# Optimization experiments

Hardware: AMD Instinct MI355X
Metric: run time of the kernel (lower is better)

Reference implementation:

```python
import jax, jax.numpy as jnp
from jax import lax
import numpy as np

T, B, H, D = 1024, 32, 8, 32
YD = 3 * D + 1
IN = H * D


def setup_inputs() -> dict:
    key = jax.random.key(0)
    ks = jax.random.split(key, 6)
    std = 1.0 / np.sqrt(D)
    return {
        "h": jax.random.normal(ks[0], (T, B, IN), jnp.float32),
        "W_y": (jax.random.normal(ks[1], (1, H, D, YD), jnp.float32) * std),
        "W_q": (jax.random.normal(ks[2], (1, H, D, D), jnp.float32) * std),
        "W_k": (jax.random.normal(ks[3], (1, H, D, D), jnp.float32) * std),
        "w_b": (jax.random.normal(ks[4], (1, H, D, 4), jnp.float32) * std),
        "W_out": (jax.random.normal(ks[5], (IN, IN), jnp.float32) / np.sqrt(IN)),
        "state_W_y": jnp.zeros((B, H, D, YD), jnp.float32),
        "state_W_q": jnp.zeros((B, H, D, D), jnp.float32),
        "state_W_k": jnp.zeros((B, H, D, D), jnp.float32),
        "state_w_b": jnp.zeros((B, H, D, 4), jnp.float32),
        "fast_weights": jnp.zeros((B, H, D, D), jnp.float32),
    }


def _srwm(x, Wy0, Wq0, Wk0, wb0):
    # Self-referential weight matrix (self_ref_v1): x time-major (T,B,H,D).
    def step(carry, x_t):
        Wy, Wq, Wk, wb = carry
        y = jnp.einsum('bhd,bhde->bhe', x_t, Wy)                      # output with W_{t-1}
        q = jax.nn.softmax(jnp.einsum('bhd,bhde->bhe', x_t, Wq), -1)
        k = jax.nn.softmax(jnp.einsum('bhd,bhde->bhe', x_t, Wk), -1)
        beta = jax.nn.sigmoid(jnp.einsum('bhd,bhde->bhe', x_t, wb))   # (B,H,4) learning rates
        def upd(M, b_i):
            vq = jnp.einsum('bhd,bhde->bhe', q, M)
            vk = jnp.einsum('bhd,bhde->bhe', k, M)
            return M + b_i[..., None, None] * k[..., :, None] * (vq - vk)[..., None, :]
        Wy = upd(Wy, beta[..., 0])
        Wq = upd(Wq, beta[..., 1])
        Wk = upd(Wk, beta[..., 2])
        wb = upd(wb, beta[..., 3])
        return (Wy, Wq, Wk, wb), y

    _, ys = lax.scan(step, (Wy0, Wq0, Wk0, wb0), x)
    return ys  # (T,B,H,YD)


def _fast_weight_memory(q, k, v, beta, F0):
    # Delta-rule fast weight memory; q,k,v (T,B,H,D), beta (T,B,H,1), F0 (B,H,D,D).
    def step(F, qkvb):
        q_t, k_t, v_t, b_t = qkvb
        v_old = jnp.einsum('bhd,bhde->bhe', k_t, F)
        F = F + b_t[..., None] * k_t[..., :, None] * (v_t - v_old)[..., None, :]
        out_t = jnp.einsum('bhd,bhde->bhe', q_t, F)
        return F, out_t

    F_fin, out = lax.scan(step, F0, (q, k, v, beta))
    return out, F_fin  # out: (T,B,H,D)


def reference(h, W_y, W_q, W_k, w_b, W_out,
              state_W_y, state_W_q, state_W_k, state_w_b, fast_weights):
    x = jax.nn.softmax(h.reshape(T, B, H, D), axis=-1)   # phi(x)
    Wy0 = state_W_y + W_y
    Wq0 = state_W_q + W_q
    Wk0 = state_W_k + W_k
    wb0 = state_w_b + w_b
    fast_qkvb = _srwm(x, Wy0, Wq0, Wk0, wb0)             # (T,B,H,3D+1)
    fq, fk, fv, fb = jnp.split(fast_qkvb, (D, 2 * D, 3 * D), axis=-1)
    fq = jax.nn.softmax(fq, -1)
    fk = jax.nn.softmax(fk, -1)
    fb = jax.nn.sigmoid(fb)
    out, _ = _fast_weight_memory(fq, fk, fv, fb, fast_weights)
    out = out.reshape(T, B, H * D)
    out = out @ W_out.T                                  # out_linear (no bias), dropout=0
    return h + out
```

## Files before the change

### kernel.cpp

```cpp
#include <hip/hip_runtime.h>
#include <cstdint>

#define TT  1024
#define BB  32
#define HH  8
#define DD  32
#define YDN 97
#define INN 256
#define BH  (BB*HH)

typedef float v2f __attribute__((ext_vector_type(2)));
typedef float v4f __attribute__((ext_vector_type(4)));

#define PK(acc, a, b) (acc) = __builtin_elementwise_fma((a), (b), (acc))

__device__ __forceinline__ void bar_lds() {
    asm volatile("s_waitcnt lgkmcnt(0)\n\ts_barrier" ::: "memory");
}
__device__ __forceinline__ void wait_lds() {
    asm volatile("s_waitcnt lgkmcnt(0)" ::: "memory");
}

template<int C>
__device__ __forceinline__ float dppf(float x) {
    return __int_as_float(__builtin_amdgcn_update_dpp(
        0, __float_as_int(x), C, 0xF, 0xF, true));
}
__device__ __forceinline__ float swz16(float x) {
    return __int_as_float(__builtin_amdgcn_ds_swizzle(__float_as_int(x), 0x401F));
}
__device__ __forceinline__ float xswap32(float v) {
    return __shfl_xor(v, 32, 64);
}
__device__ __forceinline__ float red_max32(float v) {
    v = fmaxf(v, dppf<0xB1>(v));
    v = fmaxf(v, dppf<0x4E>(v));
    v = fmaxf(v, dppf<0x141>(v));
    v = fmaxf(v, dppf<0x140>(v));
    v = fmaxf(v, swz16(v));
    return v;
}
__device__ __forceinline__ float red_sum32(float v) {
    v += dppf<0xB1>(v);
    v += dppf<0x4E>(v);
    v += dppf<0x141>(v);
    v += dppf<0x140>(v);
    v += swz16(v);
    return v;
}

__device__ __forceinline__ float cexp(float v) {
    return __expf(fminf(v, 60.f));
}

__device__ __forceinline__ float dot32(const v2f (&x)[16], const v2f (&w)[16]) {
    v2f a0 = {0.f, 0.f}, a1 = {0.f, 0.f};
    #pragma unroll
    for (int g = 0; g < 8; g++) {
        PK(a0, x[2*g],   w[2*g]);
        PK(a1, x[2*g+1], w[2*g+1]);
    }
    v2f s = a0 + a1;
    return s.x + s.y;
}

__device__ __forceinline__ void lds_read32x2(const float* a, const float* b,
                                             v2f (&ra)[16], v2f (&rb)[16]) {
    const v4f* ap = (const v4f*)a;
    const v4f* bp = (const v4f*)b;
    #pragma unroll
    for (int j = 0; j < 8; j++) {
        v4f x = ap[j]; ra[2*j] = x.xy; ra[2*j+1] = x.zw;
        v4f y = bp[j]; rb[2*j] = y.xy; rb[2*j+1] = y.zw;
    }
}

__device__ __forceinline__ void upd_row(v2f (&row2)[16], const float* u_p,
                                        const float* k_p, float beta) {
    v2f uu0[16], kk0[16];
    lds_read32x2(u_p, k_p, uu0, kk0);
    float du = dot32(uu0, row2);
    float bs = beta * du;
    v2f bs2 = {bs, bs};
    #pragma unroll
    for (int j = 0; j < 16; j++) PK(row2[j], bs2, kk0[j]);
}

__global__ __launch_bounds__(256, 1) void softmax_x_kernel(
    const float* __restrict__ hg, float* __restrict__ xg)
{
    const int row  = blockIdx.x * 8 + (threadIdx.x >> 5);
    const int lane = threadIdx.x & 31;
    float v = hg[(size_t)row * DD + lane];
    float m = red_max32(v);
    float ex = __expf(v - m);
    float sm = red_sum32(ex);
    xg[(size_t)row * DD + lane] = ex * __builtin_amdgcn_rcpf(sm);
}


#define PHASE_D(TP, P)                                                        \
    {                                                                         \
        const v4f* e4 = (const v4f*)exf_s[P];                                 \
        v2f fqh[8], fkh[8];                                                   \
        _Pragma("unroll")                                                     \
        for (int j = 0; j < 4; j++) {                                         \
            v4f a = e4[4*half + j];                                           \
            fqh[2*j] = a.xy; fqh[2*j+1] = a.zw;                               \
            v4f b = e4[8 + 4*half + j];                                       \
            fkh[2*j] = b.xy; fkh[2*j+1] = b.zw;                               \
        }                                                                     \
        float fvv = yv_s[P][l32];                                            \
        float fbp = yv_s[P][32];                                             \
                                     \
        v2f sq2 = {0.f,0.f}, sk2 = {0.f,0.f};                                 \
        _Pragma("unroll")                                                     \
        for (int j = 0; j < 8; j++) { sq2 += fqh[j]; sk2 += fkh[j]; }         \
        float sq = sq2.x + sq2.y, sk = sk2.x + sk2.y;                         \
                         \
        v2f a0 = {0.f,0.f}, a1 = {0.f,0.f};                                   \
        _Pragma("unroll")                                                     \
        for (int j = 0; j < 4; j++) {                                         \
            PK(a0, fkh[2*j],   F8[2*j]);                                      \
            PK(a1, fkh[2*j+1], F8[2*j+1]);                                    \
        }                                                                     \
        v2f vt = a0 + a1;                                                     \
        float vh = vt.x + vt.y;                                               \
        float voldr = vh + xswap32(vh);                                       \
        float sqt = sq + xswap32(sq);                                         \
        float skt = sk + xswap32(sk);                                         \
        float rrfq = __builtin_amdgcn_rcpf(sqt);                              \
        float rrfk = __builtin_amdgcn_rcpf(skt);                              \
        float fbv  = __builtin_amdgcn_rcpf(1.f + __expf(-fbp));               \
        float sup  = fbv * (fvv - rrfk * voldr) * rrfk;                       \
        v2f d2 = {sup, sup};                                                  \
        v2f o0 = {0.f,0.f}, o1 = {0.f,0.f};                                   \
        _Pragma("unroll")                                                     \
        for (int j = 0; j < 4; j++) {                                         \
            PK(F8[2*j],   d2, fkh[2*j]);   PK(o0, fqh[2*j],   F8[2*j]);       \
            PK(F8[2*j+1], d2, fkh[2*j+1]); PK(o1, fqh[2*j+1], F8[2*j+1]);     \
        }                                                                     \
        v2f ot = o0 + o1;                                                     \
        float oh = ot.x + ot.y;                                               \
        float oo = (oh + xswap32(oh)) * rrfq;                                 \
        if (lane < DD)                                                        \
            Og[((size_t)(TP) * BH + bh) * DD + lane] = oo;                    \
    }

#define PREFETCH(T, XC)                                                       \
    if ((T) + 2 < TT) {                                                       \
        const v4f* p = (const v4f*)(xg + ((size_t)((T)+2)*BH + bh)*DD);       \
        _Pragma("unroll")                                                     \
        for (int g = 0; g < 8; g++) {                                         \
            v4f v = p[g];                                                     \
            XC[2*g]   = v.xy;                                                 \
            XC[2*g+1] = v.zw;                                                 \
        }                                                                     \
    }

#define STEP_I(T, XC, P, PM)                                                  \
  {                                                                           \
    if (wv == 2) {                                                            \
        if ((T) > 0) {                                                        \
            float bb = (lane < 32) ? beta_s[PM][1] : beta_s[PM][2];           \
            float du = dot32(uu, row2);                                       \
            float bs = bb * du;                                               \
            v2f bs2 = {bs, bs};                                               \
            _Pragma("unroll")                                                 \
            for (int j = 0; j < 16; j++) PK(row2[j], bs2, kk[j]);             \
        }                                                                     \
        float pre = dot32(XC, row2);                                          \
        float ex  = cexp(pre);                                                \
        float sm  = red_sum32(ex);                                            \
        float nh  = ex * __builtin_amdgcn_rcpf(sm);                           \
        float oth = xswap32(nh);                                              \
        if (lane < DD) u_s[P][lane]      = nh - oth;                          \
        else           k_s[P][lane - DD] = nh;                                \
        wait_lds();         \
        lds_read32x2(u_s[P], k_s[P], uu, kk);                                 \
        PREFETCH(T, XC)                                                       \
    } else if (wv == 0) {                                                     \
        if ((T) > 0) upd_row(row2, u_s[PM], k_s[PM], beta_s[PM][0]);          \
        float pre = dot32(XC, row2);                                          \
        exf_s[P][lane] = cexp(pre);                                           \
        PREFETCH(T, XC)                                                       \
    } else if (wv == 1) {                                                     \
        if ((T) > 0) {                                                        \
            float bb = (lane <= 32) ? beta_s[PM][0] : beta_s[PM][3];          \
            upd_row(row2, u_s[PM], k_s[PM], bb);                              \
        }                                                                     \
        float pre = dot32(XC, row2);                                          \
        if (lane <= DD)      yv_s[P][lane] = pre;                             \
        else if (lane <= 36) beta_s[P][lane - 33] =                           \
                 __builtin_amdgcn_rcpf(1.f + __expf(-pre));                   \
        PREFETCH(T, XC)                                                       \
    } else {                                                                  \
        if ((T) > 0) { PHASE_D((T)-1, PM) }                                   \
    }                                                                         \
    bar_lds();                                                                \
  }

__global__ __launch_bounds__(256, 1) void srwm_fwm_kernel(
    const float* __restrict__ xg,
    const float* __restrict__ Wy_g, const float* __restrict__ Wq_g,
    const float* __restrict__ Wk_g, const float* __restrict__ wb_g,
    const float* __restrict__ sWy_g, const float* __restrict__ sWq_g,
    const float* __restrict__ sWk_g, const float* __restrict__ swb_g,
    const float* __restrict__ F_g,
    float* __restrict__ Og)
{
    const int bh   = blockIdx.x;
    const int hh   = bh & 7;
    const int tid  = threadIdx.x;
    const int wv   = tid >> 6;
    const int lane = tid & 63;
    const int half = lane >> 5;
    const int l32  = lane & 31;

    __shared__ __align__(16) float u_s[2][DD];
    __shared__ __align__(16) float k_s[2][DD];
    __shared__ __align__(16) float exf_s[2][64];
    __shared__ __align__(16) float yv_s[2][36];
    __shared__ __align__(16) float beta_s[2][4];

    v2f row2[16];
    v2f F8[8];
    v2f uu[16], kk[16];
    v2f XA[16], XB[16];

    if (wv < 3) {
        const float* wp = nullptr; const float* sp = nullptr; int str = 0;
        if (wv == 0) {
            wp = Wy_g  + (size_t)hh * DD * YDN + lane;
            sp = sWy_g + (size_t)bh * DD * YDN + lane;  str = YDN;
        } else if (wv == 1) {
            if (lane <= 32) {
                wp = Wy_g  + (size_t)hh * DD * YDN + 64 + lane;
                sp = sWy_g + (size_t)bh * DD * YDN + 64 + lane;  str = YDN;
            } else if (lane <= 36) {
                wp = wb_g  + (size_t)hh * DD * 4 + (lane - 33);
                sp = swb_g + (size_t)bh * DD * 4 + (lane - 33);  str = 4;
            }
        } else {
            if (lane < 32) {
                wp = Wq_g  + (size_t)hh * DD * DD + lane;
                sp = sWq_g + (size_t)bh * DD * DD + lane;
            } else {
                wp = Wk_g  + (size_t)hh * DD * DD + (lane - 32);
                sp = sWk_g + (size_t)bh * DD * DD + (lane - 32);
            }
            str = DD;
        }
        #pragma unroll
        for (int d = 0; d < 16; d++) {
            v2f t = {0.f, 0.f};
            if (wp) {
                t.x = wp[(2*d)   * str] + sp[(2*d)   * str];
                t.y = wp[(2*d+1) * str] + sp[(2*d+1) * str];
            }
            row2[d] = t;
        }
        const v4f* p0 = (const v4f*)(xg + (size_t)bh * DD);
        const v4f* p1 = (const v4f*)(xg + ((size_t)BH + bh) * DD);
        #pragma unroll
        for (int g = 0; g < 8; g++) {
            v4f a = p0[g], b = p1[g];
            XA[2*g] = a.xy; XA[2*g+1] = a.zw;
            XB[2*g] = b.xy; XB[2*g+1] = b.zw;
        }
    } else {
        const float* fp = F_g + (size_t)bh * DD * DD + (size_t)(16*half) * DD + l32;
        #pragma unroll
        for (int j = 0; j < 8; j++) {
            v2f t;
            t.x = fp[(2*j)   * DD];
            t.y = fp[(2*j+1) * DD];
            F8[j] = t;
        }
    }

    for (int t = 0; t < TT; t += 2) {
        STEP_I(t,     XA, 0, 1)
        STEP_I(t + 1, XB, 1, 0)
    }
    if (wv == 3) { PHASE_D(TT - 1, 1) }
}

#define GM 128
#define GN 128
#define GK 16

__global__ __launch_bounds__(256, 1) void out_proj_kernel(
    const float* __restrict__ O, const float* __restrict__ W,
    const float* __restrict__ hg, float* __restrict__ outg)
{
    __shared__ float As[GK][GM + 4];
    __shared__ float Bs[GK][GN + 4];
    const int tid = threadIdx.x;
    const int tx  = tid & 15;
    const int ty  = tid >> 4;
    const int r0  = blockIdx.x * GM;
    const int c0  = blockIdx.y * GN;

    float acc[8][8];
    #pragma unroll
    for (int i = 0; i < 8; i++)
        #pragma unroll
        for (int j = 0; j < 8; j++) acc[i][j] = 0.f;

    const int am = tid >> 1;
    const int ak = (tid & 1) * 8;

    for (int k0 = 0; k0 < INN; k0 += GK) {
        float4 a0 = *(const float4*)(O + (size_t)(r0 + am) * INN + k0 + ak);
        float4 a1 = *(const float4*)(O + (size_t)(r0 + am) * INN + k0 + ak + 4);
        float4 b0 = *(const float4*)(W + (size_t)(c0 + am) * INN + k0 + ak);
        float4 b1 = *(const float4*)(W + (size_t)(c0 + am) * INN + k0 + ak + 4);
        As[ak+0][am] = a0.x; As[ak+1][am] = a0.y; As[ak+2][am] = a0.z; As[ak+3][am] = a0.w;
        As[ak+4][am] = a1.x; As[ak+5][am] = a1.y; As[ak+6][am] = a1.z; As[ak+7][am] = a1.w;
        Bs[ak+0][am] = b0.x; Bs[ak+1][am] = b0.y; Bs[ak+2][am] = b0.z; Bs[ak+3][am] = b0.w;
        Bs[ak+4][am] = b1.x; Bs[ak+5][am] = b1.y; Bs[ak+6][am] = b1.z; Bs[ak+7][am] = b1.w;
        __syncthreads();
        #pragma unroll
        for (int k = 0; k < GK; k++) {
            float4 av0 = *(const float4*)&As[k][ty * 8];
            float4 av1 = *(const float4*)&As[k][ty * 8 + 4];
            float4 bv0 = *(const float4*)&Bs[k][tx * 8];
            float4 bv1 = *(const float4*)&Bs[k][tx * 8 + 4];
            float a[8] = {av0.x, av0.y, av0.z, av0.w, av1.x, av1.y, av1.z, av1.w};
            float bb[8] = {bv0.x, bv0.y, bv0.z, bv0.w, bv1.x, bv1.y, bv1.z, bv1.w};
            #pragma unroll
            for (int i = 0; i < 8; i++)
                #pragma unroll
                for (int j = 0; j < 8; j++) acc[i][j] += a[i] * bb[j];
        }
        __syncthreads();
    }

    #pragma unroll
    for (int i = 0; i < 8; i++) {
        size_t r = (size_t)(r0 + ty * 8 + i);
        float4 h0 = *(const float4*)(hg + r * INN + c0 + tx * 8);
        float4 h1 = *(const float4*)(hg + r * INN + c0 + tx * 8 + 4);
        float4 o0, o1;
        o0.x = h0.x + acc[i][0]; o0.y = h0.y + acc[i][1];
        o0.z = h0.z + acc[i][2]; o0.w = h0.w + acc[i][3];
        o1.x = h1.x + acc[i][4]; o1.y = h1.y + acc[i][5];
        o1.z = h1.z + acc[i][6]; o1.w = h1.w + acc[i][7];
        *(float4*)(outg + r * INN + c0 + tx * 8)     = o0;
        *(float4*)(outg + r * INN + c0 + tx * 8 + 4) = o1;
    }
}

extern "C" void kernel_launch(void* const* d_in, const int* in_sizes, int n_in,
                              void* d_out, int out_size, void* d_ws, size_t ws_size,
                              hipStream_t stream)
{
    (void)in_sizes; (void)n_in; (void)out_size; (void)ws_size;

    const float* hg   = (const float*)d_in[0];
    const float* Wy   = (const float*)d_in[1];
    const float* Wq   = (const float*)d_in[2];
    const float* Wk   = (const float*)d_in[3];
    const float* wb   = (const float*)d_in[4];
    const float* Wout = (const float*)d_in[5];
    const float* sWy  = (const float*)d_in[6];
    const float* sWq  = (const float*)d_in[7];
    const float* sWk  = (const float*)d_in[8];
    const float* swb  = (const float*)d_in[9];
    const float* Fw   = (const float*)d_in[10];
    float* out = (float*)d_out;

    float* xg = (float*)d_ws;
    float* Og = xg + (size_t)TT * BB * INN;

    softmax_x_kernel<<<TT * BB * HH / 8, 256, 0, stream>>>(hg, xg);
    srwm_fwm_kernel<<<BB * HH, 256, 0, stream>>>(xg, Wy, Wq, Wk, wb,
                                                 sWy, sWq, sWk, swb, Fw, Og);
    out_proj_kernel<<<dim3(TT * BB / GM, INN / GN), 256, 0, stream>>>(Og, Wout, hg, out);
}
```

Baseline: 652.4 us.

## Pipeline SRWM recurrence so wave 2 runs ahead two steps per barrier

Restructures the per-timestep SRWM/FWM schedule so wave 2 (Wq/Wk plus the wb rows it now owns) computes the q/k softmax and beta update for two timesteps between block barriers, with the other waves lagging one or two super-steps behind. Wave 2 keeps the wb learning-rate matrix in its own registers and passes unnormalized exponentials plus betas through LDS, so the other waves normalize locally. The aim is to halve the block-wide barriers and take the Wy/wb/FWM work off the critical recurrence chain. In exchange wave 2 carries extra register state and redundant per-lane sum/dot work, and the pipeline adds skew and edge-case logic at the ends of the sequence. Dot products also use four accumulators for more instruction-level parallelism.

```diff
diff --git a/kernel.cpp b/kernel.cpp
--- a/kernel.cpp
+++ b/kernel.cpp
@@ -8,6 +8,7 @@
 #define YDN 97
 #define INN 256
 #define BH  (BB*HH)
+#define NSUP (TT/2)
 
 typedef float v2f __attribute__((ext_vector_type(2)));
 typedef float v4f __attribute__((ext_vector_type(4)));
@@ -31,6 +32,9 @@
 }
 __device__ __forceinline__ float xswap32(float v) {
     return __shfl_xor(v, 32, 64);
+}
+__device__ __forceinline__ float rdlane(float v, int l) {
+    return __int_as_float(__builtin_amdgcn_readlane(__float_as_int(v), l));
 }
 __device__ __forceinline__ float red_max32(float v) {
     v = fmaxf(v, dppf<0xB1>(v));
@@ -54,13 +58,22 @@
 }
 
 __device__ __forceinline__ float dot32(const v2f (&x)[16], const v2f (&w)[16]) {
-    v2f a0 = {0.f, 0.f}, a1 = {0.f, 0.f};
+    v2f a0 = {0.f,0.f}, a1 = {0.f,0.f}, a2 = {0.f,0.f}, a3 = {0.f,0.f};
     #pragma unroll
-    for (int g = 0; g < 8; g++) {
-        PK(a0, x[2*g],   w[2*g]);
-        PK(a1, x[2*g+1], w[2*g+1]);
-    }
-    v2f s = a0 + a1;
+    for (int g = 0; g < 4; g++) {
+        PK(a0, x[4*g],   w[4*g]);
+        PK(a1, x[4*g+1], w[4*g+1]);
+        PK(a2, x[4*g+2], w[4*g+2]);
+        PK(a3, x[4*g+3], w[4*g+3]);
+    }
+    v2f s = (a0 + a1) + (a2 + a3);
+    return s.x + s.y;
+}
+
+__device__ __forceinline__ float sum32(const v2f (&q)[16]) {
+    v2f a0 = q[0]+q[1],  a1 = q[2]+q[3],  a2 = q[4]+q[5],   a3 = q[6]+q[7];
+    v2f b0 = q[8]+q[9],  b1 = q[10]+q[11],b2 = q[12]+q[13], b3 = q[14]+q[15];
+    v2f s = ((a0+a1)+(a2+a3)) + ((b0+b1)+(b2+b3));
     return s.x + s.y;
 }
 
@@ -73,17 +86,6 @@
         v4f x = ap[j]; ra[2*j] = x.xy; ra[2*j+1] = x.zw;
         v4f y = bp[j]; rb[2*j] = y.xy; rb[2*j+1] = y.zw;
     }
-}
-
-__device__ __forceinline__ void upd_row(v2f (&row2)[16], const float* u_p,
-                                        const float* k_p, float beta) {
-    v2f uu0[16], kk0[16];
-    lds_read32x2(u_p, k_p, uu0, kk0);
-    float du = dot32(uu0, row2);
-    float bs = beta * du;
-    v2f bs2 = {bs, bs};
-    #pragma unroll
-    for (int j = 0; j < 16; j++) PK(row2[j], bs2, kk0[j]);
 }
 
 __global__ __launch_bounds__(256, 1) void softmax_x_kernel(
@@ -99,9 +101,84 @@
 }
 
 
-#define PHASE_D(TP, P)                                                        \
+#define PREF(XC, S)                                                           \
     {                                                                         \
-        const v4f* e4 = (const v4f*)exf_s[P];                                 \
+        const v4f* p = (const v4f*)(xg + ((size_t)(S)*BH + bh)*DD);           \
+        _Pragma("unroll")                                                     \
+        for (int g = 0; g < 8; g++) {                                         \
+            v4f v = p[g];                                                     \
+            XC[2*g] = v.xy; XC[2*g+1] = v.zw;                                 \
+        }                                                                     \
+    }
+
+#define CORE_STEP(J, XC, P, S)                                                \
+    {                                                                         \
+        float pq = dot32(XC, row2);                                           \
+        float pw = dot32(XC, st2);                                            \
+        float ex = cexp(pq);                                                  \
+        float sg = __builtin_amdgcn_rcpf(1.f + __expf(-pw));                  \
+        ex_s[P][J][lane] = ex;                                                \
+        if (lane == 0) b_s[P][J] = sg;                                        \
+        float b1 = rdlane(sg, 1), b2 = rdlane(sg, 2), b3 = rdlane(sg, 3);     \
+        if ((S) + 2 < TT) { PREF(XC, (S)+2) }                                 \
+        wait_lds();                                                           \
+        v2f qq[16], kk[16];                                                   \
+        lds_read32x2(&ex_s[P][J][0], &ex_s[P][J][32], qq, kk);                \
+        float rrq = __builtin_amdgcn_rcpf(sum32(qq));                         \
+        float rrk = __builtin_amdgcn_rcpf(sum32(kk));                         \
+        float duq = dot32(qq, row2), duk = dot32(kk, row2);                   \
+        float du  = rrq * duq - rrk * duk;                                    \
+        float bsv = ((lane < 32) ? b1 : b2) * du * rrk;                       \
+        v2f bs2 = {bsv, bsv};                                                 \
+        _Pragma("unroll")                                                     \
+        for (int j = 0; j < 16; j++) PK(row2[j], bs2, kk[j]);                 \
+        float dq2 = dot32(qq, st2), dk2 = dot32(kk, st2);                     \
+        float du2 = rrq * dq2 - rrk * dk2;                                    \
+        float bw  = b3 * du2 * rrk;                                           \
+        v2f bw2 = {bw, bw};                                                   \
+        _Pragma("unroll")                                                     \
+        for (int j = 0; j < 16; j++) PK(st2[j], bw2, kk[j]);                  \
+    }
+
+#define W0_STEP(J, XC, PM, P, S)                                              \
+    {                                                                         \
+        v2f qq[16], kk[16];                                                   \
+        lds_read32x2(&ex_s[PM][J][0], &ex_s[PM][J][32], qq, kk);              \
+        float b0 = b_s[PM][J];                                                \
+        float pre = dot32(XC, row2);                                          \
+        exf_s[P][J][lane] = cexp(pre);                                        \
+        if ((S) + 2 < TT) { PREF(XC, (S)+2) }                                 \
+        float rrq = __builtin_amdgcn_rcpf(sum32(qq));                         \
+        float rrk = __builtin_amdgcn_rcpf(sum32(kk));                         \
+        float duq = dot32(qq, row2), duk = dot32(kk, row2);                   \
+        float du  = rrq * duq - rrk * duk;                                    \
+        float bsv = b0 * du * rrk;                                            \
+        v2f bs2 = {bsv, bsv};                                                 \
+        _Pragma("unroll")                                                     \
+        for (int j = 0; j < 16; j++) PK(row2[j], bs2, kk[j]);                 \
+    }
+
+#define W1_STEP(J, XC, PM, P, S)                                              \
+    {                                                                         \
+        v2f qq[16], kk[16];                                                   \
+        lds_read32x2(&ex_s[PM][J][0], &ex_s[PM][J][32], qq, kk);              \
+        float b0 = b_s[PM][J];                                                \
+        float pre = dot32(XC, row2);                                          \
+        if (lane <= 32) yv_s[P][J][lane] = pre;                               \
+        if ((S) + 2 < TT) { PREF(XC, (S)+2) }                                 \
+        float rrq = __builtin_amdgcn_rcpf(sum32(qq));                         \
+        float rrk = __builtin_amdgcn_rcpf(sum32(kk));                         \
+        float duq = dot32(qq, row2), duk = dot32(kk, row2);                   \
+        float du  = rrq * duq - rrk * duk;                                    \
+        float bsv = b0 * du * rrk;                                            \
+        v2f bs2 = {bsv, bsv};                                                 \
+        _Pragma("unroll")                                                     \
+        for (int j = 0; j < 16; j++) PK(row2[j], bs2, kk[j]);                 \
+    }
+
+#define D_STEP(J, PM, S)                                                      \
+    {                                                                         \
+        const v4f* e4 = (const v4f*)exf_s[PM][J];                             \
         v2f fqh[8], fkh[8];                                                   \
         _Pragma("unroll")                                                     \
         for (int j = 0; j < 4; j++) {                                         \
@@ -110,14 +187,12 @@
             v4f b = e4[8 + 4*half + j];                                       \
             fkh[2*j] = b.xy; fkh[2*j+1] = b.zw;                               \
         }                                                                     \
-        float fvv = yv_s[P][l32];                                            \
-        float fbp = yv_s[P][32];                                             \
-                                     \
+        float fvv = yv_s[PM][J][l32];                                         \
+        float fbp = yv_s[PM][J][32];                                          \
         v2f sq2 = {0.f,0.f}, sk2 = {0.f,0.f};                                 \
         _Pragma("unroll")                                                     \
         for (int j = 0; j < 8; j++) { sq2 += fqh[j]; sk2 += fkh[j]; }         \
         float sq = sq2.x + sq2.y, sk = sk2.x + sk2.y;                         \
-                         \
         v2f a0 = {0.f,0.f}, a1 = {0.f,0.f};                                   \
         _Pragma("unroll")                                                     \
         for (int j = 0; j < 4; j++) {                                         \
@@ -144,58 +219,31 @@
         float oh = ot.x + ot.y;                                               \
         float oo = (oh + xswap32(oh)) * rrfq;                                 \
         if (lane < DD)                                                        \
-            Og[((size_t)(TP) * BH + bh) * DD + lane] = oo;                    \
-    }
-
-#define PREFETCH(T, XC)                                                       \
-    if ((T) + 2 < TT) {                                                       \
-        const v4f* p = (const v4f*)(xg + ((size_t)((T)+2)*BH + bh)*DD);       \
-        _Pragma("unroll")                                                     \
-        for (int g = 0; g < 8; g++) {                                         \
-            v4f v = p[g];                                                     \
-            XC[2*g]   = v.xy;                                                 \
-            XC[2*g+1] = v.zw;                                                 \
-        }                                                                     \
-    }
-
-#define STEP_I(T, XC, P, PM)                                                  \
+            Og[((size_t)(S) * BH + bh) * DD + lane] = oo;                     \
+    }
+
+#define SUP(M, P, PM)                                                         \
   {                                                                           \
     if (wv == 2) {                                                            \
-        if ((T) > 0) {                                                        \
-            float bb = (lane < 32) ? beta_s[PM][1] : beta_s[PM][2];           \
-            float du = dot32(uu, row2);                                       \
-            float bs = bb * du;                                               \
-            v2f bs2 = {bs, bs};                                               \
-            _Pragma("unroll")                                                 \
-            for (int j = 0; j < 16; j++) PK(row2[j], bs2, kk[j]);             \
-        }                                                                     \
-        float pre = dot32(XC, row2);                                          \
-        float ex  = cexp(pre);                                                \
-        float sm  = red_sum32(ex);                                            \
-        float nh  = ex * __builtin_amdgcn_rcpf(sm);                           \
-        float oth = xswap32(nh);                                              \
-        if (lane < DD) u_s[P][lane]      = nh - oth;                          \
-        else           k_s[P][lane - DD] = nh;                                \
-        wait_lds();         \
-        lds_read32x2(u_s[P], k_s[P], uu, kk);                                 \
-        PREFETCH(T, XC)                                                       \
+        if ((M) < NSUP) {                                                     \
+            CORE_STEP(0, XA, P, 2*(M))                                        \
+            CORE_STEP(1, XB, P, 2*(M)+1)                                      \
+        }                                                                     \
     } else if (wv == 0) {                                                     \
-        if ((T) > 0) upd_row(row2, u_s[PM], k_s[PM], beta_s[PM][0]);          \
-        float pre = dot32(XC, row2);                                          \
-        exf_s[P][lane] = cexp(pre);                                           \
-        PREFETCH(T, XC)                                                       \
+        if ((M) >= 1 && (M) <= NSUP) {                                        \
+            W0_STEP(0, XA, PM, P, 2*(M)-2)                                    \
+            W0_STEP(1, XB, PM, P, 2*(M)-1)                                    \
+        }                                                                     \
     } else if (wv == 1) {                                                     \
-        if ((T) > 0) {                                                        \
-            float bb = (lane <= 32) ? beta_s[PM][0] : beta_s[PM][3];          \
-            upd_row(row2, u_s[PM], k_s[PM], bb);                              \
-        }                                                                     \
-        float pre = dot32(XC, row2);                                          \
-        if (lane <= DD)      yv_s[P][lane] = pre;                             \
-        else if (lane <= 36) beta_s[P][lane - 33] =                           \
-                 __builtin_amdgcn_rcpf(1.f + __expf(-pre));                   \
-        PREFETCH(T, XC)                                                       \
+        if ((M) >= 1 && (M) <= NSUP) {                                        \
+            W1_STEP(0, XA, PM, P, 2*(M)-2)                                    \
+            W1_STEP(1, XB, PM, P, 2*(M)-1)                                    \
+        }                                                                     \
     } else {                                                                  \
-        if ((T) > 0) { PHASE_D((T)-1, PM) }                                   \
+        if ((M) >= 2) {                                                       \
+            D_STEP(0, PM, 2*(M)-4)                                            \
+            D_STEP(1, PM, 2*(M)-3)                                            \
+        }                                                                     \
     }                                                                         \
     bar_lds();                                                                \
   }
@@ -217,16 +265,18 @@
     const int half = lane >> 5;
     const int l32  = lane & 31;
 
-    __shared__ __align__(16) float u_s[2][DD];
-    __shared__ __align__(16) float k_s[2][DD];
-    __shared__ __align__(16) float exf_s[2][64];
-    __shared__ __align__(16) float yv_s[2][36];
-    __shared__ __align__(16) float beta_s[2][4];
+    __shared__ __align__(16) float ex_s[2][2][64];
+    __shared__ __align__(16) float exf_s[2][2][64];
+    __shared__ __align__(16) float yv_s[2][2][36];
+    __shared__ __align__(16) float b_s[2][2];
 
     v2f row2[16];
+    v2f st2[16];
     v2f F8[8];
-    v2f uu[16], kk[16];
     v2f XA[16], XB[16];
+
+    #pragma unroll
+    for (int d = 0; d < 16; d++) st2[d] = (v2f){0.f, 0.f};
 
     if (wv < 3) {
         const float* wp = nullptr; const float* sp = nullptr; int str = 0;
@@ -237,9 +287,6 @@
             if (lane <= 32) {
                 wp = Wy_g  + (size_t)hh * DD * YDN + 64 + lane;
                 sp = sWy_g + (size_t)bh * DD * YDN + 64 + lane;  str = YDN;
-            } else if (lane <= 36) {
-                wp = wb_g  + (size_t)hh * DD * 4 + (lane - 33);
-                sp = swb_g + (size_t)bh * DD * 4 + (lane - 33);  str = 4;
             }
         } else {
             if (lane < 32) {
@@ -260,6 +307,17 @@
             }
             row2[d] = t;
         }
+        if (wv == 2 && lane < 4) {
+            const float* wpb = wb_g  + (size_t)hh * DD * 4 + lane;
+            const float* spb = swb_g + (size_t)bh * DD * 4 + lane;
+            #pragma unroll
+            for (int d = 0; d < 16; d++) {
+                v2f t;
+                t.x = wpb[(2*d)   * 4] + spb[(2*d)   * 4];
+                t.y = wpb[(2*d+1) * 4] + spb[(2*d+1) * 4];
+                st2[d] = t;
+            }
+        }
         const v4f* p0 = (const v4f*)(xg + (size_t)bh * DD);
         const v4f* p1 = (const v4f*)(xg + ((size_t)BH + bh) * DD);
         #pragma unroll
@@ -279,11 +337,10 @@
         }
     }
 
-    for (int t = 0; t < TT; t += 2) {
-        STEP_I(t,     XA, 0, 1)
-        STEP_I(t + 1, XB, 1, 0)
-    }
-    if (wv == 3) { PHASE_D(TT - 1, 1) }
+    for (int m = 0; m < NSUP + 2; m += 2) {
+        SUP(m,     0, 1)
+        SUP(m + 1, 1, 0)
+    }
 }
 
 #define GM 128
```

After: 1.030 ms. 1.58x slower.

## Defer softmax normalization into per-wave dots and drop cross-lane reductions

Applied to the files above, without the earlier changes.

The SRWM step no longer normalizes the q/k softmax with a wave-wide sum reduction and cross-half shuffle. It publishes unnormalized exponentials to LDS, and each wave computes the row sums and reciprocals locally from the 32-wide vectors. The pre-activation for the next step is computed algebraically as d1 + bs*dot(x,k) rather than waiting for the updated row. The fast-weight phase now runs on 32 lanes holding full rows, which removes the xor-32 shuffles. Each consumer wave does more redundant arithmetic (sums, extra dots) in exchange for a shorter serial dependency chain per step.

```diff
diff --git a/kernel.cpp b/kernel.cpp
--- a/kernel.cpp
+++ b/kernel.cpp
@@ -29,9 +29,6 @@
 __device__ __forceinline__ float swz16(float x) {
     return __int_as_float(__builtin_amdgcn_ds_swizzle(__float_as_int(x), 0x401F));
 }
-__device__ __forceinline__ float xswap32(float v) {
-    return __shfl_xor(v, 32, 64);
-}
 __device__ __forceinline__ float red_max32(float v) {
     v = fmaxf(v, dppf<0xB1>(v));
     v = fmaxf(v, dppf<0x4E>(v));
@@ -52,15 +49,27 @@
 __device__ __forceinline__ float cexp(float v) {
     return __expf(fminf(v, 60.f));
 }
+__device__ __forceinline__ float sigm(float v) {
+    return __builtin_amdgcn_rcpf(1.f + __expf(-v));
+}
 
 __device__ __forceinline__ float dot32(const v2f (&x)[16], const v2f (&w)[16]) {
-    v2f a0 = {0.f, 0.f}, a1 = {0.f, 0.f};
+    v2f a0 = {0.f,0.f}, a1 = {0.f,0.f}, a2 = {0.f,0.f}, a3 = {0.f,0.f};
     #pragma unroll
-    for (int g = 0; g < 8; g++) {
-        PK(a0, x[2*g],   w[2*g]);
-        PK(a1, x[2*g+1], w[2*g+1]);
-    }
-    v2f s = a0 + a1;
+    for (int g = 0; g < 4; g++) {
+        PK(a0, x[4*g],   w[4*g]);
+        PK(a1, x[4*g+1], w[4*g+1]);
+        PK(a2, x[4*g+2], w[4*g+2]);
+        PK(a3, x[4*g+3], w[4*g+3]);
+    }
+    v2f s = (a0 + a1) + (a2 + a3);
+    return s.x + s.y;
+}
+
+__device__ __forceinline__ float sum32(const v2f (&q)[16]) {
+    v2f a0 = q[0]+q[1],  a1 = q[2]+q[3],  a2 = q[4]+q[5],   a3 = q[6]+q[7];
+    v2f b0 = q[8]+q[9],  b1 = q[10]+q[11],b2 = q[12]+q[13], b3 = q[14]+q[15];
+    v2f s = ((a0+a1)+(a2+a3)) + ((b0+b1)+(b2+b3));
     return s.x + s.y;
 }
 
@@ -73,17 +82,6 @@
         v4f x = ap[j]; ra[2*j] = x.xy; ra[2*j+1] = x.zw;
         v4f y = bp[j]; rb[2*j] = y.xy; rb[2*j+1] = y.zw;
     }
-}
-
-__device__ __forceinline__ void upd_row(v2f (&row2)[16], const float* u_p,
-                                        const float* k_p, float beta) {
-    v2f uu0[16], kk0[16];
-    lds_read32x2(u_p, k_p, uu0, kk0);
-    float du = dot32(uu0, row2);
-    float bs = beta * du;
-    v2f bs2 = {bs, bs};
-    #pragma unroll
-    for (int j = 0; j < 16; j++) PK(row2[j], bs2, kk0[j]);
 }
 
 __global__ __launch_bounds__(256, 1) void softmax_x_kernel(
@@ -99,101 +97,90 @@
 }
 
 
-#define PHASE_D(TP, P)                                                        \
+#define PREF(XC, S)                                                           \
     {                                                                         \
-        const v4f* e4 = (const v4f*)exf_s[P];                                 \
-        v2f fqh[8], fkh[8];                                                   \
-        _Pragma("unroll")                                                     \
-        for (int j = 0; j < 4; j++) {                                         \
-            v4f a = e4[4*half + j];                                           \
-            fqh[2*j] = a.xy; fqh[2*j+1] = a.zw;                               \
-            v4f b = e4[8 + 4*half + j];                                       \
-            fkh[2*j] = b.xy; fkh[2*j+1] = b.zw;                               \
-        }                                                                     \
-        float fvv = yv_s[P][l32];                                            \
-        float fbp = yv_s[P][32];                                             \
-                                     \
-        v2f sq2 = {0.f,0.f}, sk2 = {0.f,0.f};                                 \
-        _Pragma("unroll")                                                     \
-        for (int j = 0; j < 8; j++) { sq2 += fqh[j]; sk2 += fkh[j]; }         \
-        float sq = sq2.x + sq2.y, sk = sk2.x + sk2.y;                         \
-                         \
-        v2f a0 = {0.f,0.f}, a1 = {0.f,0.f};                                   \
-        _Pragma("unroll")                                                     \
-        for (int j = 0; j < 4; j++) {                                         \
-            PK(a0, fkh[2*j],   F8[2*j]);                                      \
-            PK(a1, fkh[2*j+1], F8[2*j+1]);                                    \
-        }                                                                     \
-        v2f vt = a0 + a1;                                                     \
-        float vh = vt.x + vt.y;                                               \
-        float voldr = vh + xswap32(vh);                                       \
-        float sqt = sq + xswap32(sq);                                         \
-        float skt = sk + xswap32(sk);                                         \
-        float rrfq = __builtin_amdgcn_rcpf(sqt);                              \
-        float rrfk = __builtin_amdgcn_rcpf(skt);                              \
-        float fbv  = __builtin_amdgcn_rcpf(1.f + __expf(-fbp));               \
-        float sup  = fbv * (fvv - rrfk * voldr) * rrfk;                       \
-        v2f d2 = {sup, sup};                                                  \
-        v2f o0 = {0.f,0.f}, o1 = {0.f,0.f};                                   \
-        _Pragma("unroll")                                                     \
-        for (int j = 0; j < 4; j++) {                                         \
-            PK(F8[2*j],   d2, fkh[2*j]);   PK(o0, fqh[2*j],   F8[2*j]);       \
-            PK(F8[2*j+1], d2, fkh[2*j+1]); PK(o1, fqh[2*j+1], F8[2*j+1]);     \
-        }                                                                     \
-        v2f ot = o0 + o1;                                                     \
-        float oh = ot.x + ot.y;                                               \
-        float oo = (oh + xswap32(oh)) * rrfq;                                 \
-        if (lane < DD)                                                        \
-            Og[((size_t)(TP) * BH + bh) * DD + lane] = oo;                    \
-    }
-
-#define PREFETCH(T, XC)                                                       \
-    if ((T) + 2 < TT) {                                                       \
-        const v4f* p = (const v4f*)(xg + ((size_t)((T)+2)*BH + bh)*DD);       \
+        const v4f* p = (const v4f*)(xg + ((size_t)(S)*BH + bh)*DD);           \
         _Pragma("unroll")                                                     \
         for (int g = 0; g < 8; g++) {                                         \
             v4f v = p[g];                                                     \
-            XC[2*g]   = v.xy;                                                 \
-            XC[2*g+1] = v.zw;                                                 \
+            XC[2*g] = v.xy; XC[2*g+1] = v.zw;                                 \
         }                                                                     \
     }
 
-#define STEP_I(T, XC, P, PM)                                                  \
+#define PHASE_D(TP, PM)                                                       \
+    if (lane < 32) {                                                          \
+        v2f fqh[16], fkh[16];                                                 \
+        lds_read32x2(&exf_sh[PM][0], &exf_sh[PM][32], fqh, fkh);              \
+        float fvv = yv_sh[PM][lane];                                          \
+        float fbp = yv_sh[PM][32];                                            \
+        float fb  = sigm(fbp);                                                \
+        float rrfq = __builtin_amdgcn_rcpf(sum32(fqh));                       \
+        float rrfk = __builtin_amdgcn_rcpf(sum32(fkh));                       \
+        float vold = rrfk * dot32(fkh, F16);                                  \
+        float s    = fb * (fvv - vold) * rrfk;                                \
+        v2f s2 = {s, s};                                                      \
+        v2f o0 = {0.f,0.f}, o1 = {0.f,0.f}, o2 = {0.f,0.f}, o3 = {0.f,0.f};   \
+        _Pragma("unroll")                                                     \
+        for (int j = 0; j < 4; j++) {                                         \
+            PK(F16[4*j],   s2, fkh[4*j]);   PK(o0, fqh[4*j],   F16[4*j]);     \
+            PK(F16[4*j+1], s2, fkh[4*j+1]); PK(o1, fqh[4*j+1], F16[4*j+1]);   \
+            PK(F16[4*j+2], s2, fkh[4*j+2]); PK(o2, fqh[4*j+2], F16[4*j+2]);   \
+            PK(F16[4*j+3], s2, fkh[4*j+3]); PK(o3, fqh[4*j+3], F16[4*j+3]);   \
+        }                                                                     \
+        v2f ot = (o0 + o1) + (o2 + o3);                                       \
+        Og[((size_t)(TP) * BH + bh) * DD + lane] = (ot.x + ot.y) * rrfq;      \
+    }
+
+#define STEP(T, XC, P, PM)                                                    \
   {                                                                           \
     if (wv == 2) {                                                            \
+        float b12 = beta_s[PM][(lane < 32) ? 1 : 2];                          \
+        float d1 = dot32(XC, row2);                                           \
+        float pre;                                                            \
         if ((T) > 0) {                                                        \
-            float bb = (lane < 32) ? beta_s[PM][1] : beta_s[PM][2];           \
-            float du = dot32(uu, row2);                                       \
-            float bs = bb * du;                                               \
+            float rrq = __builtin_amdgcn_rcpf(sum32(qq));                     \
+            float rrk = __builtin_amdgcn_rcpf(sum32(kk));                     \
+            float dq  = dot32(qq, row2);                                      \
+            float dk  = dot32(kk, row2);                                      \
+            float dxk = dot32(XC, kk);                                        \
+            float du  = rrq * dq - rrk * dk;                                  \
+            float bs  = b12 * du * rrk;                                       \
+            pre = d1 + bs * dxk;                                              \
             v2f bs2 = {bs, bs};                                               \
             _Pragma("unroll")                                                 \
             for (int j = 0; j < 16; j++) PK(row2[j], bs2, kk[j]);             \
+        } else pre = d1;                                                      \
+        ex_sh[P][lane] = cexp(pre);                                           \
+        if ((T) + 2 < TT) { PREF(XC, (T) + 2) }                               \
+        wait_lds();                     \
+        lds_read32x2(&ex_sh[P][0], &ex_sh[P][32], qq, kk);                    \
+    } else if (wv < 2) {                                                      \
+        v2f qr[16], kr[16];                                                   \
+        lds_read32x2(&ex_sh[PM][0], &ex_sh[PM][32], qr, kr);                  \
+        float b0 = (wv == 0) ? beta_s[PM][0]                                  \
+                 : ((lane <= 32) ? beta_s[PM][0] : beta_s[PM][3]);            \
+        float d1 = dot32(XC, row2);                                           \
+        float pre;                                                            \
+        if ((T) > 0) {                                                        \
+            float rrq = __builtin_amdgcn_rcpf(sum32(qr));                     \
+            float rrk = __builtin_amdgcn_rcpf(sum32(kr));                     \
+            float dq  = dot32(qr, row2);                                      \
+            float dk  = dot32(kr, row2);                                      \
+            float dxk = dot32(XC, kr);                                        \
+            float du  = rrq * dq - rrk * dk;                                  \
+            float bs  = b0 * du * rrk;                                        \
+            pre = d1 + bs * dxk;                                              \
+            v2f bs2 = {bs, bs};                                               \
+            _Pragma("unroll")                                                 \
+            for (int j = 0; j < 16; j++) PK(row2[j], bs2, kr[j]);             \
+        } else pre = d1;                                                      \
+        if (wv == 0) {                                                        \
+            exf_sh[P][lane] = cexp(pre);                                      \
+        } else {                                                              \
+            if (lane <= 32)      yv_sh[P][lane] = pre;                        \
+            else if (lane <= 36) beta_s[P][lane - 33] = sigm(pre);            \
         }                                                                     \
-        float pre = dot32(XC, row2);                                          \
-        float ex  = cexp(pre);                                                \
-        float sm  = red_sum32(ex);                                            \
-        float nh  = ex * __builtin_amdgcn_rcpf(sm);                           \
-        float oth = xswap32(nh);                                              \
-        if (lane < DD) u_s[P][lane]      = nh - oth;                          \
-        else           k_s[P][lane - DD] = nh;                                \
-        wait_lds();         \
-        lds_read32x2(u_s[P], k_s[P], uu, kk);                                 \
-        PREFETCH(T, XC)                                                       \
-    } else if (wv == 0) {                                                     \
-        if ((T) > 0) upd_row(row2, u_s[PM], k_s[PM], beta_s[PM][0]);          \
-        float pre = dot32(XC, row2);                                          \
-        exf_s[P][lane] = cexp(pre);                                           \
-        PREFETCH(T, XC)                                                       \
-    } else if (wv == 1) {                                                     \
-        if ((T) > 0) {                                                        \
-            float bb = (lane <= 32) ? beta_s[PM][0] : beta_s[PM][3];          \
-            upd_row(row2, u_s[PM], k_s[PM], bb);                              \
-        }                                                                     \
-        float pre = dot32(XC, row2);                                          \
-        if (lane <= DD)      yv_s[P][lane] = pre;                             \
-        else if (lane <= 36) beta_s[P][lane - 33] =                           \
-                 __builtin_amdgcn_rcpf(1.f + __expf(-pre));                   \
-        PREFETCH(T, XC)                                                       \
+        if ((T) + 2 < TT) { PREF(XC, (T) + 2) }                               \
     } else {                                                                  \
         if ((T) > 0) { PHASE_D((T)-1, PM) }                                   \
     }                                                                         \
@@ -214,18 +201,15 @@
     const int tid  = threadIdx.x;
     const int wv   = tid >> 6;
     const int lane = tid & 63;
-    const int half = lane >> 5;
-    const int l32  = lane & 31;
-
-    __shared__ __align__(16) float u_s[2][DD];
-    __shared__ __align__(16) float k_s[2][DD];
-    __shared__ __align__(16) float exf_s[2][64];
-    __shared__ __align__(16) float yv_s[2][36];
+
+    __shared__ __align__(16) float ex_sh[2][64];
+    __shared__ __align__(16) float exf_sh[2][64];
+    __shared__ __align__(16) float yv_sh[2][36];
     __shared__ __align__(16) float beta_s[2][4];
 
     v2f row2[16];
-    v2f F8[8];
-    v2f uu[16], kk[16];
+    v2f F16[16];
+    v2f qq[16], kk[16];
     v2f XA[16], XB[16];
 
     if (wv < 3) {
@@ -269,19 +253,21 @@
             XB[2*g] = b.xy; XB[2*g+1] = b.zw;
         }
     } else {
-        const float* fp = F_g + (size_t)bh * DD * DD + (size_t)(16*half) * DD + l32;
-        #pragma unroll
-        for (int j = 0; j < 8; j++) {
-            v2f t;
-            t.x = fp[(2*j)   * DD];
-            t.y = fp[(2*j+1) * DD];
-            F8[j] = t;
+        if (lane < 32) {
+            const float* fp = F_g + (size_t)bh * DD * DD + lane;
+            #pragma unroll
+            for (int d = 0; d < 16; d++) {
+                v2f t;
+                t.x = fp[(2*d)   * DD];
+                t.y = fp[(2*d+1) * DD];
+                F16[d] = t;
+            }
         }
     }
 
     for (int t = 0; t < TT; t += 2) {
-        STEP_I(t,     XA, 0, 1)
-        STEP_I(t + 1, XB, 1, 0)
+        STEP(t,     XA, 0, 1)
+        STEP(t + 1, XB, 1, 0)
     }
     if (wv == 3) { PHASE_D(TT - 1, 1) }
 }
```

New measurement: 768.5 us. 17.8% more time.
